# Kernel tuning notes

Hardware: AMD Instinct MI355X
Metric: run time of the kernel (lower is better)

The kernel has to match this reference:

```python
import jax, jax.numpy as jnp
import numpy as np

E = 600000
N = 50000
H = 128
OE = 256


def swish(v):
    return v * jax.nn.sigmoid(v)


def setup_inputs() -> dict:
    key = jax.random.key(0)
    ks = jax.random.split(key, 16)
    inp = {
        "x": jax.random.normal(ks[0], (E, H), dtype=jnp.float32),
        "rbf": jax.random.normal(ks[1], (E, 6), dtype=jnp.float32),
        "i": jax.random.randint(ks[2], (E,), 0, N, dtype=jnp.int32),
        "edge_index": jax.random.randint(ks[3], (2, E), 0, N, dtype=jnp.int32),
        "edge_weight": jax.random.uniform(ks[4], (E,), dtype=jnp.float32),
        "batch": jax.random.randint(ks[5], (N,), 0, 32, dtype=jnp.int32),
        "num_nodes": N,
        "W_rbf": jax.random.normal(ks[6], (H, 6), dtype=jnp.float32) * 0.2,
        "W_up": jax.random.normal(ks[7], (OE, H), dtype=jnp.float32) * (1.0 / np.sqrt(H)),
        "b_up": jnp.zeros((OE,), dtype=jnp.float32),
        "W_l1": jax.random.normal(ks[8], (OE, OE), dtype=jnp.float32) * (1.0 / np.sqrt(OE)),
        "b_l1": jnp.zeros((OE,), dtype=jnp.float32),
        "W_l2": jax.random.normal(ks[9], (OE, OE), dtype=jnp.float32) * (1.0 / np.sqrt(OE)),
        "b_l2": jnp.zeros((OE,), dtype=jnp.float32),
        "W_l3": jax.random.normal(ks[10], (OE, OE), dtype=jnp.float32) * (1.0 / np.sqrt(OE)),
        "b_l3": jnp.zeros((OE,), dtype=jnp.float32),
        "W_out": jax.random.normal(ks[11], (1, OE), dtype=jnp.float32) * (1.0 / np.sqrt(OE)),
        "W_w": jax.random.normal(ks[12], (1, H), dtype=jnp.float32) * (1.0 / np.sqrt(H)),
        "b_w": jnp.zeros((1,), dtype=jnp.float32),
    }
    return inp


def reference(x, rbf, i, edge_index, edge_weight, batch, num_nodes,
              W_rbf, W_up, b_up, W_l1, b_l1, W_l2, b_l2, W_l3, b_l3,
              W_out, W_w, b_w):
    # edge_index / edge_weight are unused in the original forward.
    # x = lin_rbf(rbf) * x  -> [E, H]
    xe = (rbf @ W_rbf.T) * x
    # scatter-add edges -> nodes: [N, H]
    xn = jax.ops.segment_sum(xe, i, num_segments=num_nodes)
    # energy head: alpha = w_lin(x) before lin_up
    alpha = xn @ W_w.T + b_w  # [N, 1]
    x2 = xn @ W_up.T + b_up   # [N, OE]
    for W, b in ((W_l1, b_l1), (W_l2, b_l2), (W_l3, b_l3)):
        x2 = swish(x2 @ W.T + b)
    out = (x2 @ W_out.T) * alpha  # [N, 1]
    return (out, batch)
```

## Files before the change

### kernel.cpp

```cpp
#include <hip/hip_runtime.h>
#include <hip/hip_bf16.h>
#include <math.h>

#define E_CNT 600000
#define N_CNT 50000
#define H_DIM 128
#define OE_DIM 256

typedef __attribute__((ext_vector_type(8))) short short8;
typedef __attribute__((ext_vector_type(4))) float f32x4;

#define WS_EIDS   0
#define WS_OFF    2400000
#define WS_CURS   2600008
#define WS_CNT    2800008
#define WS_WUP    3000016
#define WS_WL1    3065552
#define WS_WL2    3196624
#define WS_WL3    3327696
#define WS_TEXC   3500000
#define WS_BSUM   3700704

#define SCAN_NB 196
#define WCONV_NB 896

__global__ __launch_bounds__(256) void histwconv_kernel(
    const int* __restrict__ nid, int* __restrict__ counts,
    const float* __restrict__ Wup, const float* __restrict__ Wl1,
    const float* __restrict__ Wl2, const float* __restrict__ Wl3,
    ushort* __restrict__ dUp, ushort* __restrict__ dL1,
    ushort* __restrict__ dL2, ushort* __restrict__ dL3)
{
    if (blockIdx.x < WCONV_NB) {
        int d = blockIdx.x * 256 + threadIdx.x;
        const float* W;
        ushort* dst;
        int K;
        if (d < 32768)       { W = Wup; dst = dUp; K = 128; }
        else if (d < 98304)  { d -= 32768;  W = Wl1; dst = dL1; K = 256; }
        else if (d < 163840) { d -= 98304;  W = Wl2; dst = dL2; K = 256; }
        else                 { d -= 163840; W = Wl3; dst = dL3; K = 256; }
        int j = d & 7;
        int l = (d >> 3) & 63;
        int KS = K >> 5;
        int ks = (d >> 9) % KS;
        int ot = (d >> 9) / KS;
        int k = ks * 32 + ((l >> 4) << 3) + j;
        int o = ot * 16 + (l & 15);
        __hip_bfloat16 h = __float2bfloat16(W[o * K + k]);
        dst[d] = *(const ushort*)&h;
    } else {
        int nb = gridDim.x - WCONV_NB;
        for (int e = (blockIdx.x - WCONV_NB) * 256 + threadIdx.x; e < E_CNT;
             e += nb * 256)
            atomicAdd(&counts[nid[e]], 1);
    }
}

__global__ __launch_bounds__(256) void scanA_kernel(const int* __restrict__ counts,
                                                    int* __restrict__ texc,
                                                    int* __restrict__ bsum)
{
    __shared__ int s[256];
    const int t = threadIdx.x;
    const int i = blockIdx.x * 256 + t;
    int v = (i < N_CNT) ? counts[i] : 0;
    s[t] = v;
    __syncthreads();
    for (int off = 1; off < 256; off <<= 1) {
        int u = (t >= off) ? s[t - off] : 0;
        __syncthreads();
        s[t] += u;
        __syncthreads();
    }
    texc[i] = s[t] - v;
    if (t == 255) bsum[blockIdx.x] = s[255];
}

__global__ __launch_bounds__(256) void scanC_kernel(const int* __restrict__ texc,
                                                    const int* __restrict__ bsum,
                                                    int* __restrict__ offs,
                                                    int* __restrict__ cursor)
{
    __shared__ int red[256];
    const int t = threadIdx.x;
    int v = (t < (int)blockIdx.x && t < SCAN_NB) ? bsum[t] : 0;
    red[t] = v;
    __syncthreads();
    for (int off = 128; off >= 1; off >>= 1) {
        if (t < off) red[t] += red[t + off];
        __syncthreads();
    }
    const int boff = red[0];
    const int i = blockIdx.x * 256 + t;
    if (i < N_CNT) {
        int o = texc[i] + boff;
        offs[i] = o;
        cursor[i] = o;
    }
    if (i == 0) offs[N_CNT] = E_CNT;
}

__global__ __launch_bounds__(256) void fill_kernel(const int* __restrict__ nid,
                                                   int* __restrict__ cursor,
                                                   int* __restrict__ eids)
{
    for (int e = blockIdx.x * 256 + threadIdx.x; e < E_CNT; e += gridDim.x * 256) {
        int slot = atomicAdd(&cursor[nid[e]], 1);
        eids[slot] = e;
    }
}

#define MB 32
#define PITCH 264
#define EMAX 640

template<int KS, bool SW>
__device__ __forceinline__ void layer(const ushort* __restrict__ Wsh,
                                      const float* __restrict__ bias,
                                      const ushort* in_s, ushort* out_s, int tid)
{
    const int w = tid >> 6, lane = tid & 63;
    const int l15 = lane & 15, lg = lane >> 4;

    f32x4 acc[2][2];
#pragma unroll
    for (int mi = 0; mi < 2; ++mi)
#pragma unroll
        for (int oi = 0; oi < 2; ++oi)
            acc[mi][oi] = (f32x4){0.f, 0.f, 0.f, 0.f};

#pragma unroll
    for (int ks = 0; ks < KS; ++ks) {
        short8 b0 = *(const short8*)(Wsh + (size_t)(((w * 2 + 0) * KS + ks) * 64 + lane) * 8);
        short8 b1 = *(const short8*)(Wsh + (size_t)(((w * 2 + 1) * KS + ks) * 64 + lane) * 8);
#pragma unroll
        for (int mi = 0; mi < 2; ++mi) {
            short8 a = *(const short8*)(in_s + (mi * 16 + l15) * PITCH + ks * 32 + lg * 8);
            acc[mi][0] = __builtin_amdgcn_mfma_f32_16x16x32_bf16(a, b0, acc[mi][0], 0, 0, 0);
            acc[mi][1] = __builtin_amdgcn_mfma_f32_16x16x32_bf16(a, b1, acc[mi][1], 0, 0, 0);
        }
    }

#pragma unroll
    for (int oi = 0; oi < 2; ++oi) {
        float bv = bias[(w * 2 + oi) * 16 + l15];
#pragma unroll
        for (int mi = 0; mi < 2; ++mi)
#pragma unroll
            for (int r = 0; r < 4; ++r) {
                float v = acc[mi][oi][r] + bv;
                if (SW) v = v / (1.f + __expf(-v));
                __hip_bfloat16 h = __float2bfloat16(v);
                out_s[(mi * 16 + lg * 4 + r) * PITCH + (w * 2 + oi) * 16 + l15] =
                    *(const ushort*)&h;
            }
    }
}

__global__ __launch_bounds__(512, 4) void fused_kernel(
    const float* __restrict__ x, const float* __restrict__ rbf,
    const int* __restrict__ offs, const int* __restrict__ eids,
    const float* __restrict__ W_rbf, const float* __restrict__ W_w,
    const float* __restrict__ b_w,
    const ushort* __restrict__ Wup, const ushort* __restrict__ Wl1,
    const ushort* __restrict__ Wl2, const ushort* __restrict__ Wl3,
    const float* __restrict__ b_up, const float* __restrict__ b_l1,
    const float* __restrict__ b_l2, const float* __restrict__ b_l3,
    const float* __restrict__ W_out, const int* __restrict__ batch,
    float* __restrict__ out)
{
    __shared__ ushort sA[MB * PITCH];
    __shared__ ushort sB[MB * PITCH];
    __shared__ int s_eids[EMAX];
    __shared__ int s_off[MB + 1];
    __shared__ float s_alpha[MB];

    const int tid = threadIdx.x;
    const int w = tid >> 6, lane = tid & 63;
    const int node0 = blockIdx.x * MB;

    if (tid < MB) {
        int node = node0 + tid;
        if (node < N_CNT) out[N_CNT + node] = (float)batch[node];
    }
    if (tid < MB + 1)
        s_off[tid] = offs[min(node0 + tid, N_CNT)];
    __syncthreads();

    const int s0 = s_off[0];
    const int tot = s_off[MB] - s0;
    const int nchunks = (tot + EMAX - 1) / EMAX;

    {
        const int half = lane >> 5;
        const int hb = (lane & 31) * 4;
        float wrb[4][6];
#pragma unroll
        for (int j = 0; j < 4; ++j)
#pragma unroll
            for (int k = 0; k < 6; ++k)
                wrb[j][k] = W_rbf[(hb + j) * 6 + k];
        float ww[4];
#pragma unroll
        for (int j = 0; j < 4; ++j) ww[j] = W_w[hb + j];
        const float bw = b_w[0];

        for (int c = 0; c < nchunks; ++c) {
            const int cs = c * EMAX;
            const int ce = min(cs + EMAX, tot);
            __syncthreads();
            for (int t = tid + cs; t < ce; t += 512) s_eids[t - cs] = eids[s0 + t];
            __syncthreads();

            for (int nl4 = 0; nl4 < 4; ++nl4) {
                const int nl = (w << 2) + nl4;
                const int ls = max(s_off[nl] - s0, cs);
                const int le = min(s_off[nl + 1] - s0, ce);
                float a0 = 0.f, a1 = 0.f, a2 = 0.f, a3 = 0.f;

                int i = ls;
                float4 xv_n = make_float4(0.f, 0.f, 0.f, 0.f);
                float2 q0n = make_float2(0.f, 0.f), q1n = q0n, q2n = q0n;
                if (i + 1 < le) {
                    const int ee = s_eids[i - cs + half];
                    xv_n = *(const float4*)(x + (size_t)ee * H_DIM + hb);
                    const float2* rp = (const float2*)(rbf + (size_t)ee * 6);
                    q0n = rp[0]; q1n = rp[1]; q2n = rp[2];
                }
                for (; i + 1 < le; ) {
                    const float4 xv = xv_n;
                    const float2 q0 = q0n, q1 = q1n, q2 = q2n;
                    i += 2;
                    if (i + 1 < le) {
                        const int ee = s_eids[i - cs + half];
                        xv_n = *(const float4*)(x + (size_t)ee * H_DIM + hb);
                        const float2* rp = (const float2*)(rbf + (size_t)ee * 6);
                        q0n = rp[0]; q1n = rp[1]; q2n = rp[2];
                    }
                    const float r[6] = {q0.x, q0.y, q1.x, q1.y, q2.x, q2.y};
                    float c0 = 0.f, c1 = 0.f, c2 = 0.f, c3 = 0.f;
#pragma unroll
                    for (int k = 0; k < 6; ++k) {
                        c0 = fmaf(r[k], wrb[0][k], c0);
                        c1 = fmaf(r[k], wrb[1][k], c1);
                        c2 = fmaf(r[k], wrb[2][k], c2);
                        c3 = fmaf(r[k], wrb[3][k], c3);
                    }
                    a0 = fmaf(c0, xv.x, a0);
                    a1 = fmaf(c1, xv.y, a1);
                    a2 = fmaf(c2, xv.z, a2);
                    a3 = fmaf(c3, xv.w, a3);
                }
                if (i < le && half == 0) {
                    const int ee = s_eids[i - cs];
                    const float4 xv = *(const float4*)(x + (size_t)ee * H_DIM + hb);
                    const float2* rp = (const float2*)(rbf + (size_t)ee * 6);
                    const float2 q0 = rp[0], q1 = rp[1], q2 = rp[2];
                    const float r[6] = {q0.x, q0.y, q1.x, q1.y, q2.x, q2.y};
                    float c0 = 0.f, c1 = 0.f, c2 = 0.f, c3 = 0.f;
#pragma unroll
                    for (int k = 0; k < 6; ++k) {
                        c0 = fmaf(r[k], wrb[0][k], c0);
                        c1 = fmaf(r[k], wrb[1][k], c1);
                        c2 = fmaf(r[k], wrb[2][k], c2);
                        c3 = fmaf(r[k], wrb[3][k], c3);
                    }
                    a0 = fmaf(c0, xv.x, a0);
                    a1 = fmaf(c1, xv.y, a1);
                    a2 = fmaf(c2, xv.z, a2);
                    a3 = fmaf(c3, xv.w, a3);
                }

                a0 += __shfl_xor(a0, 32);
                a1 += __shfl_xor(a1, 32);
                a2 += __shfl_xor(a2, 32);
                a3 += __shfl_xor(a3, 32);

                if (half == 0) {
                    ushort4* dp = (ushort4*)(sA + nl * PITCH + hb);
                    if (c > 0) {
                        ushort4 old = *dp;
                        a0 += __bfloat162float(*(const __hip_bfloat16*)&old.x);
                        a1 += __bfloat162float(*(const __hip_bfloat16*)&old.y);
                        a2 += __bfloat162float(*(const __hip_bfloat16*)&old.z);
                        a3 += __bfloat162float(*(const __hip_bfloat16*)&old.w);
                    }
                    __hip_bfloat16 h0 = __float2bfloat16(a0), h1 = __float2bfloat16(a1);
                    __hip_bfloat16 h2 = __float2bfloat16(a2), h3 = __float2bfloat16(a3);
                    ushort4 pk;
                    pk.x = *(const ushort*)&h0;
                    pk.y = *(const ushort*)&h1;
                    pk.z = *(const ushort*)&h2;
                    pk.w = *(const ushort*)&h3;
                    *dp = pk;
                }

                float part = fmaf(a0, ww[0], fmaf(a1, ww[1], fmaf(a2, ww[2], a3 * ww[3])));
                part += __shfl_xor(part, 1);
                part += __shfl_xor(part, 2);
                part += __shfl_xor(part, 4);
                part += __shfl_xor(part, 8);
                part += __shfl_xor(part, 16);
                if (lane == 0) {
                    if (c > 0) s_alpha[nl] += part;
                    else       s_alpha[nl] = part + bw;
                }
            }
        }
    }
    __syncthreads();

    layer<4, false>(Wup, b_up, sA, sB, tid);
    __syncthreads();
    layer<8, true>(Wl1, b_l1, sB, sA, tid);
    __syncthreads();
    layer<8, true>(Wl2, b_l2, sA, sB, tid);
    __syncthreads();
    layer<8, true>(Wl3, b_l3, sB, sA, tid);
    __syncthreads();

    {
        int nl = tid >> 4, q = tid & 15;
        const ushort* rowp = sA + nl * PITCH + q * 16;
        float sum = 0.f;
#pragma unroll
        for (int o = 0; o < 16; ++o) {
            __hip_bfloat16 h = *(const __hip_bfloat16*)(rowp + o);
            sum = fmaf(__bfloat162float(h), W_out[q * 16 + o], sum);
        }
        sum += __shfl_xor(sum, 1);
        sum += __shfl_xor(sum, 2);
        sum += __shfl_xor(sum, 4);
        sum += __shfl_xor(sum, 8);
        int node = node0 + nl;
        if (q == 0 && node < N_CNT) out[node] = sum * s_alpha[nl];
    }
}

extern "C" void kernel_launch(void* const* d_in, const int* in_sizes, int n_in,
                              void* d_out, int out_size, void* d_ws, size_t ws_size,
                              hipStream_t stream)
{
    const float* x      = (const float*)d_in[0];
    const float* rbf    = (const float*)d_in[1];
    const int*   nid    = (const int*)d_in[2];
    const int*   batch  = (const int*)d_in[5];
    const float* W_rbf  = (const float*)d_in[7];
    const float* W_up   = (const float*)d_in[8];
    const float* b_up   = (const float*)d_in[9];
    const float* W_l1   = (const float*)d_in[10];
    const float* b_l1   = (const float*)d_in[11];
    const float* W_l2   = (const float*)d_in[12];
    const float* b_l2   = (const float*)d_in[13];
    const float* W_l3   = (const float*)d_in[14];
    const float* b_l3   = (const float*)d_in[15];
    const float* W_out  = (const float*)d_in[16];
    const float* W_w    = (const float*)d_in[17];
    const float* b_w    = (const float*)d_in[18];

    char* ws = (char*)d_ws;
    int*    eids   = (int*)(ws + WS_EIDS);
    int*    offs   = (int*)(ws + WS_OFF);
    int*    cursor = (int*)(ws + WS_CURS);
    int*    counts = (int*)(ws + WS_CNT);
    ushort* WupS   = (ushort*)(ws + WS_WUP);
    ushort* Wl1S   = (ushort*)(ws + WS_WL1);
    ushort* Wl2S   = (ushort*)(ws + WS_WL2);
    ushort* Wl3S   = (ushort*)(ws + WS_WL3);
    int*    texc   = (int*)(ws + WS_TEXC);
    int*    bsum   = (int*)(ws + WS_BSUM);
    float*  out    = (float*)d_out;

    hipMemsetAsync(counts, 0, N_CNT * sizeof(int), stream);
    histwconv_kernel<<<WCONV_NB + 1024, 256, 0, stream>>>(
        nid, counts, W_up, W_l1, W_l2, W_l3, WupS, Wl1S, Wl2S, Wl3S);
    scanA_kernel<<<SCAN_NB, 256, 0, stream>>>(counts, texc, bsum);
    scanC_kernel<<<SCAN_NB, 256, 0, stream>>>(texc, bsum, offs, cursor);
    fill_kernel<<<1024, 256, 0, stream>>>(nid, cursor, eids);

    fused_kernel<<<(N_CNT + MB - 1) / MB, 512, 0, stream>>>(
        x, rbf, offs, eids, W_rbf, W_w, b_w,
        WupS, Wl1S, Wl2S, Wl3S, b_up, b_l1, b_l2, b_l3, W_out, batch, out);
}
```

Measured before the change: 228.6 us.

## Precompute bf16 edge features in sorted order during fill, stream them in fused kernel

```diff
diff --git a/kernel.cpp b/kernel.cpp
--- a/kernel.cpp
+++ b/kernel.cpp
@@ -10,16 +10,16 @@
 typedef __attribute__((ext_vector_type(8))) short short8;
 typedef __attribute__((ext_vector_type(4))) float f32x4;
 
-#define WS_EIDS   0
-#define WS_OFF    2400000
-#define WS_CURS   2600008
-#define WS_CNT    2800008
-#define WS_WUP    3000016
-#define WS_WL1    3065552
-#define WS_WL2    3196624
-#define WS_WL3    3327696
-#define WS_TEXC   3500000
-#define WS_BSUM   3700704
+#define WS_OFF    0
+#define WS_CURS   200008
+#define WS_CNT    400008
+#define WS_TEXC   600008
+#define WS_BSUM   800712
+#define WS_WUP    801736
+#define WS_WL1    867272
+#define WS_WL2    998344
+#define WS_WL3    1129416
+#define WS_XE     1261568
 
 #define SCAN_NB 196
 #define WCONV_NB 896
@@ -101,19 +101,62 @@
     if (i == 0) offs[N_CNT] = E_CNT;
 }
 
-__global__ __launch_bounds__(256) void fill_kernel(const int* __restrict__ nid,
-                                                   int* __restrict__ cursor,
-                                                   int* __restrict__ eids)
-{
-    for (int e = blockIdx.x * 256 + threadIdx.x; e < E_CNT; e += gridDim.x * 256) {
-        int slot = atomicAdd(&cursor[nid[e]], 1);
-        eids[slot] = e;
+__global__ __launch_bounds__(256, 4) void prepass_kernel(
+    const float* __restrict__ x, const float* __restrict__ rbf,
+    const int* __restrict__ nid, int* __restrict__ cursor,
+    const float* __restrict__ W_rbf,
+    ushort* __restrict__ xep)
+{
+    const int tid = threadIdx.x;
+    const int lane = tid & 63;
+    const int half = lane >> 5;
+    const int l31 = lane & 31;
+    const int h0 = l31 * 4;
+
+    float wrb[4][6];
+#pragma unroll
+    for (int j = 0; j < 4; ++j)
+#pragma unroll
+        for (int k = 0; k < 6; ++k)
+            wrb[j][k] = W_rbf[(h0 + j) * 6 + k];
+
+    const int wid = (blockIdx.x * 256 + tid) >> 6;
+    const int nw = (gridDim.x * 256) >> 6;
+    const int npair = E_CNT / 2;
+
+    for (int p = wid; p < npair; p += nw) {
+        const int e = p * 2 + half;
+        const int node = nid[e];
+        int slot = 0;
+        if (l31 == 0) slot = atomicAdd(&cursor[node], 1);
+        slot = __shfl(slot, half << 5);
+
+        const float4 xv = *(const float4*)(x + (size_t)e * H_DIM + h0);
+        const float2* rp = (const float2*)(rbf + (size_t)e * 6);
+        const float2 q0 = rp[0], q1 = rp[1], q2 = rp[2];
+        const float r[6] = {q0.x, q0.y, q1.x, q1.y, q2.x, q2.y};
+        float c0 = 0.f, c1 = 0.f, c2 = 0.f, c3 = 0.f;
+#pragma unroll
+        for (int k = 0; k < 6; ++k) {
+            c0 = fmaf(r[k], wrb[0][k], c0);
+            c1 = fmaf(r[k], wrb[1][k], c1);
+            c2 = fmaf(r[k], wrb[2][k], c2);
+            c3 = fmaf(r[k], wrb[3][k], c3);
+        }
+        const float v0 = c0 * xv.x, v1 = c1 * xv.y, v2 = c2 * xv.z, v3 = c3 * xv.w;
+        __hip_bfloat16 b0 = __float2bfloat16(v0), b1 = __float2bfloat16(v1);
+        __hip_bfloat16 b2 = __float2bfloat16(v2), b3 = __float2bfloat16(v3);
+        ushort4 pk;
+        pk.x = *(const ushort*)&b0;
+        pk.y = *(const ushort*)&b1;
+        pk.z = *(const ushort*)&b2;
+        pk.w = *(const ushort*)&b3;
+        *(ushort4*)(xep + (size_t)slot * H_DIM + h0) = pk;
     }
 }
 
 #define MB 32
 #define PITCH 264
-#define EMAX 640
 
 template<int KS, bool SW>
 __device__ __forceinline__ void layer(const ushort* __restrict__ Wsh,
@@ -158,11 +201,10 @@
     }
 }
 
-__global__ __launch_bounds__(512, 4) void fused_kernel(
-    const float* __restrict__ x, const float* __restrict__ rbf,
-    const int* __restrict__ offs, const int* __restrict__ eids,
-    const float* __restrict__ W_rbf, const float* __restrict__ W_w,
-    const float* __restrict__ b_w,
+__global__ __launch_bounds__(512, 6) void fused_kernel(
+    const ushort* __restrict__ xep,
+    const int* __restrict__ offs,
+    const float* __restrict__ W_w, const float* __restrict__ b_w,
     const ushort* __restrict__ Wup, const ushort* __restrict__ Wl1,
     const ushort* __restrict__ Wl2, const ushort* __restrict__ Wl3,
     const float* __restrict__ b_up, const float* __restrict__ b_l1,
@@ -172,7 +214,6 @@
 {
     __shared__ ushort sA[MB * PITCH];
     __shared__ ushort sB[MB * PITCH];
-    __shared__ int s_eids[EMAX];
     __shared__ int s_off[MB + 1];
     __shared__ float s_alpha[MB];
 
@@ -188,124 +229,51 @@
         s_off[tid] = offs[min(node0 + tid, N_CNT)];
     __syncthreads();
 
-    const int s0 = s_off[0];
-    const int tot = s_off[MB] - s0;
-    const int nchunks = (tot + EMAX - 1) / EMAX;
-
     {
-        const int half = lane >> 5;
-        const int hb = (lane & 31) * 4;
-        float wrb[4][6];
-#pragma unroll
-        for (int j = 0; j < 4; ++j)
-#pragma unroll
-            for (int k = 0; k < 6; ++k)
-                wrb[j][k] = W_rbf[(hb + j) * 6 + k];
-        float ww[4];
-#pragma unroll
-        for (int j = 0; j < 4; ++j) ww[j] = W_w[hb + j];
+        const int eq = lane >> 4;
+        const int p = lane & 15;
+        float ww[8];
+#pragma unroll
+        for (int j = 0; j < 8; ++j) ww[j] = W_w[p * 8 + j];
         const float bw = b_w[0];
 
-        for (int c = 0; c < nchunks; ++c) {
-            const int cs = c * EMAX;
-            const int ce = min(cs + EMAX, tot);
-            __syncthreads();
-            for (int t = tid + cs; t < ce; t += 512) s_eids[t - cs] = eids[s0 + t];
-            __syncthreads();
-
-            for (int nl4 = 0; nl4 < 4; ++nl4) {
-                const int nl = (w << 2) + nl4;
-                const int ls = max(s_off[nl] - s0, cs);
-                const int le = min(s_off[nl + 1] - s0, ce);
-                float a0 = 0.f, a1 = 0.f, a2 = 0.f, a3 = 0.f;
-
-                int i = ls;
-                float4 xv_n = make_float4(0.f, 0.f, 0.f, 0.f);
-                float2 q0n = make_float2(0.f, 0.f), q1n = q0n, q2n = q0n;
-                if (i + 1 < le) {
-                    const int ee = s_eids[i - cs + half];
-                    xv_n = *(const float4*)(x + (size_t)ee * H_DIM + hb);
-                    const float2* rp = (const float2*)(rbf + (size_t)ee * 6);
-                    q0n = rp[0]; q1n = rp[1]; q2n = rp[2];
+        for (int nl4 = 0; nl4 < 4; ++nl4) {
+            const int nl = (w << 2) + nl4;
+            const int ls = s_off[nl], le = s_off[nl + 1];
+            float acc[8];
+#pragma unroll
+            for (int j = 0; j < 8; ++j) acc[j] = 0.f;
+
+#pragma unroll 2
+            for (int s = ls + eq; s < le; s += 4) {
+                short8 rv = *(const short8*)(xep + (size_t)s * H_DIM + p * 8);
+#pragma unroll
+                for (int j = 0; j < 8; ++j) {
+                    ushort u = (ushort)rv[j];
+                    acc[j] += __bfloat162float(*(const __hip_bfloat16*)&u);
                 }
-                for (; i + 1 < le; ) {
-                    const float4 xv = xv_n;
-                    const float2 q0 = q0n, q1 = q1n, q2 = q2n;
-                    i += 2;
-                    if (i + 1 < le) {
-                        const int ee = s_eids[i - cs + half];
-                        xv_n = *(const float4*)(x + (size_t)ee * H_DIM + hb);
-                        const float2* rp = (const float2*)(rbf + (size_t)ee * 6);
-                        q0n = rp[0]; q1n = rp[1]; q2n = rp[2];
-                    }
-                    const float r[6] = {q0.x, q0.y, q1.x, q1.y, q2.x, q2.y};
-                    float c0 = 0.f, c1 = 0.f, c2 = 0.f, c3 = 0.f;
-#pragma unroll
-                    for (int k = 0; k < 6; ++k) {
-                        c0 = fmaf(r[k], wrb[0][k], c0);
-                        c1 = fmaf(r[k], wrb[1][k], c1);
-                        c2 = fmaf(r[k], wrb[2][k], c2);
-                        c3 = fmaf(r[k], wrb[3][k], c3);
-                    }
-                    a0 = fmaf(c0, xv.x, a0);
-                    a1 = fmaf(c1, xv.y, a1);
-                    a2 = fmaf(c2, xv.z, a2);
-                    a3 = fmaf(c3, xv.w, a3);
+            }
+#pragma unroll
+            for (int j = 0; j < 8; ++j) {
+                acc[j] += __shfl_xor(acc[j], 16);
+                acc[j] += __shfl_xor(acc[j], 32);
+            }
+            float part = 0.f;
+#pragma unroll
+            for (int j = 0; j < 8; ++j) part = fmaf(acc[j], ww[j], part);
+            part += __shfl_xor(part, 1);
+            part += __shfl_xor(part, 2);
+            part += __shfl_xor(part, 4);
+            part += __shfl_xor(part, 8);
+            if (lane == 0) s_alpha[nl] = part + bw;
+            if (eq == 0) {
+                ushort pk[8];
+#pragma unroll
+                for (int j = 0; j < 8; ++j) {
+                    __hip_bfloat16 h = __float2bfloat16(acc[j]);
+                    pk[j] = *(const ushort*)&h;
                 }
-                if (i < le && half == 0) {
-                    const int ee = s_eids[i - cs];
-                    const float4 xv = *(const float4*)(x + (size_t)ee * H_DIM + hb);
-                    const float2* rp = (const float2*)(rbf + (size_t)ee * 6);
-                    const float2 q0 = rp[0], q1 = rp[1], q2 = rp[2];
-                    const float r[6] = {q0.x, q0.y, q1.x, q1.y, q2.x, q2.y};
-                    float c0 = 0.f, c1 = 0.f, c2 = 0.f, c3 = 0.f;
-#pragma unroll
-                    for (int k = 0; k < 6; ++k) {
-                        c0 = fmaf(r[k], wrb[0][k], c0);
-                        c1 = fmaf(r[k], wrb[1][k], c1);
-                        c2 = fmaf(r[k], wrb[2][k], c2);
-                        c3 = fmaf(r[k], wrb[3][k], c3);
-                    }
-                    a0 = fmaf(c0, xv.x, a0);
-                    a1 = fmaf(c1, xv.y, a1);
-                    a2 = fmaf(c2, xv.z, a2);
-                    a3 = fmaf(c3, xv.w, a3);
-                }
-
-                a0 += __shfl_xor(a0, 32);
-                a1 += __shfl_xor(a1, 32);
-                a2 += __shfl_xor(a2, 32);
-                a3 += __shfl_xor(a3, 32);
-
-                if (half == 0) {
-                    ushort4* dp = (ushort4*)(sA + nl * PITCH + hb);
-                    if (c > 0) {
-                        ushort4 old = *dp;
-                        a0 += __bfloat162float(*(const __hip_bfloat16*)&old.x);
-                        a1 += __bfloat162float(*(const __hip_bfloat16*)&old.y);
-                        a2 += __bfloat162float(*(const __hip_bfloat16*)&old.z);
-                        a3 += __bfloat162float(*(const __hip_bfloat16*)&old.w);
-                    }
-                    __hip_bfloat16 h0 = __float2bfloat16(a0), h1 = __float2bfloat16(a1);
-                    __hip_bfloat16 h2 = __float2bfloat16(a2), h3 = __float2bfloat16(a3);
-                    ushort4 pk;
-                    pk.x = *(const ushort*)&h0;
-                    pk.y = *(const ushort*)&h1;
-                    pk.z = *(const ushort*)&h2;
-                    pk.w = *(const ushort*)&h3;
-                    *dp = pk;
-                }
-
-                float part = fmaf(a0, ww[0], fmaf(a1, ww[1], fmaf(a2, ww[2], a3 * ww[3])));
-                part += __shfl_xor(part, 1);
-                part += __shfl_xor(part, 2);
-                part += __shfl_xor(part, 4);
-                part += __shfl_xor(part, 8);
-                part += __shfl_xor(part, 16);
-                if (lane == 0) {
-                    if (c > 0) s_alpha[nl] += part;
-                    else       s_alpha[nl] = part + bw;
-                }
+                *(int4*)(sA + nl * PITCH + p * 8) = *(const int4*)pk;
             }
         }
     }
@@ -360,16 +328,16 @@
     const float* b_w    = (const float*)d_in[18];
 
     char* ws = (char*)d_ws;
-    int*    eids   = (int*)(ws + WS_EIDS);
     int*    offs   = (int*)(ws + WS_OFF);
     int*    cursor = (int*)(ws + WS_CURS);
     int*    counts = (int*)(ws + WS_CNT);
+    int*    texc   = (int*)(ws + WS_TEXC);
+    int*    bsum   = (int*)(ws + WS_BSUM);
     ushort* WupS   = (ushort*)(ws + WS_WUP);
     ushort* Wl1S   = (ushort*)(ws + WS_WL1);
     ushort* Wl2S   = (ushort*)(ws + WS_WL2);
     ushort* Wl3S   = (ushort*)(ws + WS_WL3);
-    int*    texc   = (int*)(ws + WS_TEXC);
-    int*    bsum   = (int*)(ws + WS_BSUM);
+    ushort* xep    = (ushort*)(ws + WS_XE);
     float*  out    = (float*)d_out;
 
     hipMemsetAsync(counts, 0, N_CNT * sizeof(int), stream);
@@ -377,9 +345,10 @@
         nid, counts, W_up, W_l1, W_l2, W_l3, WupS, Wl1S, Wl2S, Wl3S);
     scanA_kernel<<<SCAN_NB, 256, 0, stream>>>(counts, texc, bsum);
     scanC_kernel<<<SCAN_NB, 256, 0, stream>>>(texc, bsum, offs, cursor);
-    fill_kernel<<<1024, 256, 0, stream>>>(nid, cursor, eids);
+
+    prepass_kernel<<<2048, 256, 0, stream>>>(x, rbf, nid, cursor, W_rbf, xep);
 
     fused_kernel<<<(N_CNT + MB - 1) / MB, 512, 0, stream>>>(
-        x, rbf, offs, eids, W_rbf, W_w, b_w,
+        xep, offs, W_w, b_w,
         WupS, Wl1S, Wl2S, Wl3S, b_up, b_l1, b_l2, b_l3, W_out, batch, out);
 }
```

Result: faster. 219.7 us (-3.9%).
